# Kernel optimization log

Measured on AMD Instinct MI355X. Metric: run time of the kernel, lower is better.

The kernel has to match this reference:

```python
import jax, jax.numpy as jnp
import numpy as np

DIM = 2048
NUM_HEADS = 16
HEAD_DIM = DIM // NUM_HEADS  # 128


def setup_inputs() -> dict:
    key = jax.random.key(0)
    ks = jax.random.split(key, 5)
    scale = 0.02
    x = jax.random.normal(ks[0], (1, 2048, DIM), dtype=jnp.float32)
    # nn.Linear weights stored as [out_features, in_features]
    Wq = jax.random.normal(ks[1], (DIM, DIM), dtype=jnp.float32) * scale
    Wk = jax.random.normal(ks[2], (HEAD_DIM, DIM), dtype=jnp.float32) * scale
    Wv = jax.random.normal(ks[3], (HEAD_DIM, DIM), dtype=jnp.float32) * scale
    Wo = jax.random.normal(ks[4], (DIM, DIM), dtype=jnp.float32) * scale
    return {"x": x, "Wq": Wq, "Wk": Wk, "Wv": Wv, "Wo": Wo}


def reference(x, Wq, Wk, Wv, Wo):
    batch, seq_len, dim = x.shape
    q = x @ Wq.T                                   # [b, s, dim]
    k = x @ Wk.T                                   # [b, s, head_dim] (shared across heads)
    v = x @ Wv.T                                   # [b, s, head_dim]
    q = q.reshape(batch, seq_len, NUM_HEADS, HEAD_DIM).transpose(0, 2, 1, 3)  # [b, h, s, d]
    # MQA: single KV head broadcast across query heads (no materialized repeat)
    scores = jnp.einsum("bhqd,bkd->bhqk", q, k) / (HEAD_DIM ** 0.5)
    probs = jax.nn.softmax(scores, axis=-1)        # [b, h, q, k]
    out = jnp.einsum("bhqk,bkd->bhqd", probs, v)   # [b, h, s, d]
    out = out.transpose(0, 2, 1, 3).reshape(batch, seq_len, dim)
    return out @ Wo.T
```

## Files before the change

### kernel.cpp

```cpp
#include <hip/hip_runtime.h>
#include <cmath>

typedef float    float4_t __attribute__((ext_vector_type(4)));
typedef float    f32x16   __attribute__((ext_vector_type(16)));
typedef __bf16   bf16x8   __attribute__((ext_vector_type(8)));
typedef unsigned uint4_v  __attribute__((ext_vector_type(4)));
typedef unsigned short u16;

__device__ __forceinline__ u16 f2bf(float f) {
    unsigned u = __float_as_uint(f);
    u += 0x7fffu + ((u >> 16) & 1u);
    return (u16)(u >> 16);
}

__device__ __forceinline__ unsigned cvtpk(float a, float b) {
    unsigned r;
    asm("v_cvt_pk_bf16_f32 %0, %1, %2" : "=v"(r) : "v"(a), "v"(b));
    return r;
}
__device__ __forceinline__ void pl32swap(unsigned& a, unsigned& b) {
    asm volatile("v_permlane32_swap_b32 %0, %1" : "+v"(a), "+v"(b));
}

#define GLOAD_LDS16(g, l)                                              \
    __builtin_amdgcn_global_load_lds(                                  \
        (__attribute__((address_space(1))) void*)(g),                  \
        (__attribute__((address_space(3))) void*)(l), 16, 0, 0)

__device__ __forceinline__ int sw_st(int cs, int row) { return ((cs - (row >> 1)) & 3) * 8; }
__device__ __forceinline__ int sw_rd(int ch, int row) { return (((ch + (row >> 1)) & 3)) * 8; }

__global__ __launch_bounds__(256) void cast_all(const float* __restrict__ x,
                                                const float* __restrict__ wq,
                                                const float* __restrict__ wk,
                                                const float* __restrict__ wv,
                                                const float* __restrict__ wo,
                                                u16* __restrict__ xb, u16* __restrict__ wqb,
                                                u16* __restrict__ wkb, u16* __restrict__ wvb,
                                                u16* __restrict__ wob) {
    const int b = blockIdx.x;
    const float* src;
    u16* dst;
    int i;
    if (b < 4096)      { src = x;  dst = xb;  i = b * 256 + threadIdx.x; }
    else if (b < 8192) { src = wq; dst = wqb; i = (b - 4096) * 256 + threadIdx.x; }
    else if (b < 8448) { src = wk; dst = wkb; i = (b - 8192) * 256 + threadIdx.x; }
    else if (b < 8704) { src = wv; dst = wvb; i = (b - 8448) * 256 + threadIdx.x; }
    else               { src = wo; dst = wob; i = (b - 8704) * 256 + threadIdx.x; }
    float4 f = ((const float4*)src)[i];
    ushort4 r;
    r.x = f2bf(f.x); r.y = f2bf(f.y); r.z = f2bf(f.z); r.w = f2bf(f.w);
    ((ushort4*)dst)[i] = r;
}

template <typename EPI>
__device__ __forceinline__ void gemm_core(const u16* __restrict__ A,
                                          const u16* __restrict__ B,
                                          int K, int bm, int bn, EPI epi) {
    __shared__ __align__(16) u16 As[2][2 * 64 * 32];
    __shared__ __align__(16) u16 Bs[2][2 * 128 * 32];
    const int tid  = threadIdx.x;
    const int lane = tid & 63, wave = tid >> 6;
    const int quad = lane >> 4, l16 = lane & 15;

    float4_t acc[4][2] = {};

    auto stage = [&](int k0, int buf) {
#pragma unroll
        for (int i = 0; i < 2; ++i) {
            const int slot = i * 256 + tid;
            const int ksb = slot >> 8, win = slot & 255;
            const int row = win >> 2;
            GLOAD_LDS16(A + (size_t)(bm + row) * K + k0 + ksb * 32 + sw_st(win & 3, row),
                        &As[buf][slot * 8]);
        }
#pragma unroll
        for (int i = 0; i < 4; ++i) {
            const int slot = i * 256 + tid;
            const int ksb = slot >> 9, win = slot & 511;
            const int row = win >> 2;
            GLOAD_LDS16(B + (size_t)(bn + row) * K + k0 + ksb * 32 + sw_st(win & 3, row),
                        &Bs[buf][slot * 8]);
        }
    };

    stage(0, 0);
    __syncthreads();
    int cur = 0;
    for (int k0 = 0; k0 < K; k0 += 64) {
        if (k0 + 64 < K) stage(k0 + 64, cur ^ 1);

        bf16x8 af[2][4], bfr[2][2];
#pragma unroll
        for (int ksb = 0; ksb < 2; ++ksb) {
#pragma unroll
            for (int mi = 0; mi < 4; ++mi) {
                const int rw = mi * 16 + l16;
                af[ksb][mi] = *(const bf16x8*)&As[cur][ksb * 2048 + rw * 32 + sw_rd(quad, rw)];
            }
#pragma unroll
            for (int ni = 0; ni < 2; ++ni) {
                const int rw = wave * 32 + ni * 16 + l16;
                bfr[ksb][ni] = *(const bf16x8*)&Bs[cur][ksb * 4096 + rw * 32 + sw_rd(quad, rw)];
            }
        }
#pragma unroll
        for (int mi = 0; mi < 4; ++mi)
#pragma unroll
            for (int ni = 0; ni < 2; ++ni) {
                acc[mi][ni] = __builtin_amdgcn_mfma_f32_16x16x32_bf16(
                    af[0][mi], bfr[0][ni], acc[mi][ni], 0, 0, 0);
                acc[mi][ni] = __builtin_amdgcn_mfma_f32_16x16x32_bf16(
                    af[1][mi], bfr[1][ni], acc[mi][ni], 0, 0, 0);
            }
        __syncthreads();
        cur ^= 1;
    }

#pragma unroll
    for (int mi = 0; mi < 4; ++mi) {
        const int row = bm + mi * 16 + quad * 4;
#pragma unroll
        for (int ni = 0; ni < 2; ++ni) {
            const int col = bn + wave * 32 + ni * 16 + l16;
#pragma unroll
            for (int r = 0; r < 4; ++r) epi(row + r, col, acc[mi][ni][r]);
        }
    }
}

__global__ __launch_bounds__(256) void gemm_qkv(const u16* __restrict__ A,
                                                const u16* __restrict__ B,
                                                u16* __restrict__ qb,
                                                u16* __restrict__ kb,
                                                u16* __restrict__ vtb) {
    gemm_core(A, B, 2048, blockIdx.x * 64, blockIdx.y * 128,
              [=](int row, int col, float v) {
                  if (col < 2048)
                      qb[(size_t)row * 2048 + col] = f2bf(v * 0.1275174313451427f);
                  else if (col < 2176)
                      kb[(size_t)row * 128 + (col - 2048)] = f2bf(v);
                  else
                      vtb[(size_t)(col - 2176) * 2048 + row] = f2bf(v);
              });
}

__global__ __launch_bounds__(256) void gemm_out(const u16* __restrict__ A,
                                                const u16* __restrict__ B,
                                                float* __restrict__ C) {
    gemm_core(A, B, 2048, blockIdx.x * 64, blockIdx.y * 128,
              [=](int row, int col, float v) {
                  C[(size_t)row * 2048 + col] = v;
              });
}

__global__ __launch_bounds__(256) void mqa_attn(const u16* __restrict__ Q,
                                                const u16* __restrict__ Kmat,
                                                const u16* __restrict__ Vt,
                                                float* __restrict__ Oacc0,
                                                float* __restrict__ Oacc1,
                                                float* __restrict__ Lsum) {
    __shared__ __align__(16) u16 Ks[2][4 * 64 * 32];
    __shared__ __align__(16) u16 Vts[2][2 * 128 * 32];
    const int tid  = threadIdx.x;
    const int wave = tid >> 6, lane = tid & 63;
    const int l31 = lane & 31, hi = lane >> 5;
    const int h     = blockIdx.y;
    const int ksp   = blockIdx.z;
    const int qbase = blockIdx.x * 128 + wave * 32;
    const int kbase = ksp * 1024;

    bf16x8 qf[8];
    {
        const u16* qptr = Q + (size_t)(qbase + l31) * 2048 + h * 128 + hi * 8;
#pragma unroll
        for (int c = 0; c < 8; ++c) qf[c] = *(const bf16x8*)(qptr + c * 16);
    }

    f32x16 acc[4];
#pragma unroll
    for (int dt = 0; dt < 4; ++dt) acc[dt] = (f32x16)(0.0f);
    float lsum = 0.f;

    auto stage = [&](int s, int buf) {
        const int k0 = kbase + s * 64;
#pragma unroll
        for (int i = 0; i < 4; ++i) {
            const int slot = i * 256 + tid;
            const int kb4 = slot >> 8, win = slot & 255;
            const int row = win >> 2;
            GLOAD_LDS16(Kmat + (size_t)(k0 + row) * 128 + kb4 * 32 + sw_st(win & 3, row),
                        &Ks[buf][slot * 8]);
        }
#pragma unroll
        for (int i = 0; i < 4; ++i) {
            const int slot = i * 256 + tid;
            const int kk = slot >> 9, win = slot & 511;
            const int row = win >> 2;
            GLOAD_LDS16(Vt + (size_t)row * 2048 + k0 + kk * 32 + sw_st(win & 3, row),
                        &Vts[buf][slot * 8]);
        }
    };

    stage(0, 0);
    __syncthreads();
    int cur = 0;

    for (int s = 0; s < 16; ++s) {
        if (s < 15) stage(s + 1, cur ^ 1);

        bf16x8 pa[4];
#pragma unroll
        for (int kt = 0; kt < 2; ++kt) {
            f32x16 sv = (f32x16)(0.0f);
            const int row = kt * 32 + l31;
#pragma unroll
            for (int c = 0; c < 8; ++c) {
                const int ch = (c & 1) * 2 + hi;
                bf16x8 kf = *(const bf16x8*)&Ks[cur][(c >> 1) * 2048 + row * 32 + sw_rd(ch, row)];
                sv = __builtin_amdgcn_mfma_f32_32x32x16_bf16(kf, qf[c], sv, 0, 0, 0);
            }
            float e[16];
#pragma unroll
            for (int r = 0; r < 16; ++r) {
                e[r] = exp2f(sv[r]);
                lsum += e[r];
            }
#pragma unroll
            for (int half = 0; half < 2; ++half) {
                unsigned a0 = cvtpk(e[half * 8 + 0], e[half * 8 + 1]);
                unsigned a1 = cvtpk(e[half * 8 + 2], e[half * 8 + 3]);
                unsigned b0 = cvtpk(e[half * 8 + 4], e[half * 8 + 5]);
                unsigned b1 = cvtpk(e[half * 8 + 6], e[half * 8 + 7]);
                pl32swap(a0, b0);
                pl32swap(a1, b1);
                uint4_v w = {a0, a1, b0, b1};
                pa[kt * 2 + half] = __builtin_bit_cast(bf16x8, w);
            }
        }

#pragma unroll
        for (int kc = 0; kc < 4; ++kc) {
            const int ch = (kc & 1) * 2 + hi;
            const int kk = kc >> 1;
#pragma unroll
            for (int dt = 0; dt < 4; ++dt) {
                const int row = dt * 32 + l31;
                bf16x8 vf = *(const bf16x8*)&Vts[cur][kk * 4096 + row * 32 + sw_rd(ch, row)];
                acc[dt] = __builtin_amdgcn_mfma_f32_32x32x16_bf16(pa[kc], vf, acc[dt], 0, 0, 0);
            }
        }
        __syncthreads();
        cur ^= 1;
    }

    float lrow = lsum + __shfl_xor(lsum, 32);
    float* __restrict__ Op = ksp ? Oacc1 : Oacc0;
    if (lane < 32) Lsum[(size_t)ksp * 32768 + h * 2048 + qbase + l31] = lrow;
#pragma unroll
    for (int dt = 0; dt < 4; ++dt)
#pragma unroll
        for (int r = 0; r < 16; ++r) {
            const int qloc = (r & 3) + 8 * (r >> 2) + 4 * hi;
            Op[((size_t)h * 2048 + qbase + qloc) * 128 + dt * 32 + l31] = acc[dt][r];
        }
}

__global__ __launch_bounds__(256) void attn_combine(const float* __restrict__ O0,
                                                    const float* __restrict__ O1,
                                                    const float* __restrict__ L,
                                                    u16* __restrict__ attn) {
    const int f = blockIdx.x * 256 + threadIdx.x;
    const int d4 = f & 31, h = (f >> 5) & 15, q = f >> 9;
    const int li = h * 2048 + q;
    const float inv = 1.0f / (L[li] + L[32768 + li]);
    const int oi = li * 32 + d4;
    const float4 a = ((const float4*)O0)[oi];
    const float4 b = ((const float4*)O1)[oi];
    ushort4 r;
    r.x = f2bf((a.x + b.x) * inv);
    r.y = f2bf((a.y + b.y) * inv);
    r.z = f2bf((a.z + b.z) * inv);
    r.w = f2bf((a.w + b.w) * inv);
    ((ushort4*)attn)[f] = r;
}

extern "C" void kernel_launch(void* const* d_in, const int* in_sizes, int n_in,
                              void* d_out, int out_size, void* d_ws, size_t ws_size,
                              hipStream_t stream) {
    const float* x  = (const float*)d_in[0];
    const float* Wq = (const float*)d_in[1];
    const float* Wk = (const float*)d_in[2];
    const float* Wv = (const float*)d_in[3];
    const float* Wo = (const float*)d_in[4];
    float* out = (float*)d_out;

    u16* ws   = (u16*)d_ws;
    u16* xb   = ws;
    u16* Wqb  = xb  + (4 << 20);
    u16* Wkb  = Wqb + (4 << 20);
    u16* Wvb  = Wkb + (256 << 10);
    u16* Wob  = Wvb + (256 << 10);
    u16* qb   = Wob + (4 << 20);
    u16* kb   = qb  + (4 << 20);
    u16* vtb  = kb  + (256 << 10);
    u16* attn = vtb + (256 << 10);
    float* Oacc0 = (float*)ws;
    float* Oacc1 = (float*)(attn + (4 << 20));
    float* Lsum  = Oacc1 + (4 << 20);

    cast_all<<<12800, 256, 0, stream>>>(x, Wq, Wk, Wv, Wo, xb, Wqb, Wkb, Wvb, Wob);

    gemm_qkv<<<dim3(32, 18), 256, 0, stream>>>(xb, Wqb, qb, kb, vtb);
    mqa_attn<<<dim3(16, 16, 2), 256, 0, stream>>>(qb, kb, vtb, Oacc0, Oacc1, Lsum);
    attn_combine<<<4096, 256, 0, stream>>>(Oacc0, Oacc1, Lsum, attn);
    gemm_out<<<dim3(32, 16), 256, 0, stream>>>(attn, Wob, out);
}
```

Baseline: 219.0 us.

## Read K and V^T directly from global memory in MQA attention, dropping LDS staging

The attention kernel no longer stages K and V^T tiles through double-buffered shared memory with barriers. Each wave instead loads its MFMA operands straight from global memory, relying on L2/cache reuse since the single shared KV head is small. V^T is written with a padded row stride (2112) so that strided global reads avoid channel or bank conflicts, and the workspace is enlarged to fit it. This removes LDS traffic and __syncthreads, but exposes global-load latency with no explicit prefetch beyond unrolling by two.

New measurement: 309.5 us. 1.41x slower.

```diff
diff --git a/kernel.cpp b/kernel.cpp
--- a/kernel.cpp
+++ b/kernel.cpp
@@ -6,6 +6,8 @@
 typedef __bf16   bf16x8   __attribute__((ext_vector_type(8)));
 typedef unsigned uint4_v  __attribute__((ext_vector_type(4)));
 typedef unsigned short u16;
+
+#define VSTR 2112
 
 __device__ __forceinline__ u16 f2bf(float f) {
     unsigned u = __float_as_uint(f);
@@ -141,7 +143,7 @@
                   else if (col < 2176)
                       kb[(size_t)row * 128 + (col - 2048)] = f2bf(v);
                   else
-                      vtb[(size_t)(col - 2176) * 2048 + row] = f2bf(v);
+                      vtb[(size_t)(col - 2176) * VSTR + row] = f2bf(v);
               });
 }
 
@@ -160,8 +162,6 @@
                                                 float* __restrict__ Oacc0,
                                                 float* __restrict__ Oacc1,
                                                 float* __restrict__ Lsum) {
-    __shared__ __align__(16) u16 Ks[2][4 * 64 * 32];
-    __shared__ __align__(16) u16 Vts[2][2 * 128 * 32];
     const int tid  = threadIdx.x;
     const int wave = tid >> 6, lane = tid & 63;
     const int l31 = lane & 31, hi = lane >> 5;
@@ -182,42 +182,18 @@
     for (int dt = 0; dt < 4; ++dt) acc[dt] = (f32x16)(0.0f);
     float lsum = 0.f;
 
-    auto stage = [&](int s, int buf) {
+#pragma unroll 2
+    for (int s = 0; s < 16; ++s) {
         const int k0 = kbase + s * 64;
-#pragma unroll
-        for (int i = 0; i < 4; ++i) {
-            const int slot = i * 256 + tid;
-            const int kb4 = slot >> 8, win = slot & 255;
-            const int row = win >> 2;
-            GLOAD_LDS16(Kmat + (size_t)(k0 + row) * 128 + kb4 * 32 + sw_st(win & 3, row),
-                        &Ks[buf][slot * 8]);
-        }
-#pragma unroll
-        for (int i = 0; i < 4; ++i) {
-            const int slot = i * 256 + tid;
-            const int kk = slot >> 9, win = slot & 511;
-            const int row = win >> 2;
-            GLOAD_LDS16(Vt + (size_t)row * 2048 + k0 + kk * 32 + sw_st(win & 3, row),
-                        &Vts[buf][slot * 8]);
-        }
-    };
-
-    stage(0, 0);
-    __syncthreads();
-    int cur = 0;
-
-    for (int s = 0; s < 16; ++s) {
-        if (s < 15) stage(s + 1, cur ^ 1);
 
         bf16x8 pa[4];
 #pragma unroll
         for (int kt = 0; kt < 2; ++kt) {
             f32x16 sv = (f32x16)(0.0f);
-            const int row = kt * 32 + l31;
+            const u16* kp = Kmat + (size_t)(k0 + kt * 32 + l31) * 128 + hi * 8;
 #pragma unroll
             for (int c = 0; c < 8; ++c) {
-                const int ch = (c & 1) * 2 + hi;
-                bf16x8 kf = *(const bf16x8*)&Ks[cur][(c >> 1) * 2048 + row * 32 + sw_rd(ch, row)];
+                bf16x8 kf = *(const bf16x8*)(kp + c * 16);
                 sv = __builtin_amdgcn_mfma_f32_32x32x16_bf16(kf, qf[c], sv, 0, 0, 0);
             }
             float e[16];
@@ -240,18 +216,14 @@
         }
 
 #pragma unroll
-        for (int kc = 0; kc < 4; ++kc) {
-            const int ch = (kc & 1) * 2 + hi;
-            const int kk = kc >> 1;
-#pragma unroll
-            for (int dt = 0; dt < 4; ++dt) {
-                const int row = dt * 32 + l31;
-                bf16x8 vf = *(const bf16x8*)&Vts[cur][kk * 4096 + row * 32 + sw_rd(ch, row)];
+        for (int dt = 0; dt < 4; ++dt) {
+            const u16* vp = Vt + (size_t)(dt * 32 + l31) * VSTR + k0 + hi * 8;
+#pragma unroll
+            for (int kc = 0; kc < 4; ++kc) {
+                bf16x8 vf = *(const bf16x8*)(vp + kc * 16);
                 acc[dt] = __builtin_amdgcn_mfma_f32_32x32x16_bf16(pa[kc], vf, acc[dt], 0, 0, 0);
             }
         }
-        __syncthreads();
-        cur ^= 1;
     }
 
     float lrow = lsum + __shfl_xor(lsum, 32);
@@ -304,7 +276,7 @@
     u16* qb   = Wob + (4 << 20);
     u16* kb   = qb  + (4 << 20);
     u16* vtb  = kb  + (256 << 10);
-    u16* attn = vtb + (256 << 10);
+    u16* attn = vtb + (512 << 10);
     float* Oacc0 = (float*)ws;
     float* Oacc1 = (float*)(attn + (4 << 20));
     float* Lsum  = Oacc1 + (4 << 20);
```

## Process two query tiles per wave in MQA attention and pad V^T stride

Applied to the files above, without the earlier changes.

Each wave now handles 64 query rows (two 32-row tiles) instead of 32, so every K and V fragment read from LDS feeds two MFMAs. The block shrinks to 128 threads (2 waves) while keeping the same 128-query tile, and staging loops are doubled to compensate. V^T rows are padded to a stride of 2112 to reduce channel/bank conflicts on the global loads. This roughly doubles register pressure per wave (accumulators and Q fragments) and halves waves per block, which risks lower occupancy and less latency hiding.

After: 238.7 us. +9.0%, slower.

```diff
diff --git a/kernel.cpp b/kernel.cpp
--- a/kernel.cpp
+++ b/kernel.cpp
@@ -6,6 +6,8 @@
 typedef __bf16   bf16x8   __attribute__((ext_vector_type(8)));
 typedef unsigned uint4_v  __attribute__((ext_vector_type(4)));
 typedef unsigned short u16;
+
+#define VSTR 2112
 
 __device__ __forceinline__ u16 f2bf(float f) {
     unsigned u = __float_as_uint(f);
@@ -141,7 +143,7 @@
                   else if (col < 2176)
                       kb[(size_t)row * 128 + (col - 2048)] = f2bf(v);
                   else
-                      vtb[(size_t)(col - 2176) * 2048 + row] = f2bf(v);
+                      vtb[(size_t)(col - 2176) * VSTR + row] = f2bf(v);
               });
 }
 
@@ -154,12 +156,12 @@
               });
 }
 
-__global__ __launch_bounds__(256) void mqa_attn(const u16* __restrict__ Q,
-                                                const u16* __restrict__ Kmat,
-                                                const u16* __restrict__ Vt,
-                                                float* __restrict__ Oacc0,
-                                                float* __restrict__ Oacc1,
-                                                float* __restrict__ Lsum) {
+__global__ __launch_bounds__(128, 1) void mqa_attn(const u16* __restrict__ Q,
+                                                   const u16* __restrict__ Kmat,
+                                                   const u16* __restrict__ Vt,
+                                                   float* __restrict__ Oacc0,
+                                                   float* __restrict__ Oacc1,
+                                                   float* __restrict__ Lsum) {
     __shared__ __align__(16) u16 Ks[2][4 * 64 * 32];
     __shared__ __align__(16) u16 Vts[2][2 * 128 * 32];
     const int tid  = threadIdx.x;
@@ -167,37 +169,40 @@
     const int l31 = lane & 31, hi = lane >> 5;
     const int h     = blockIdx.y;
     const int ksp   = blockIdx.z;
-    const int qbase = blockIdx.x * 128 + wave * 32;
+    const int qbase = blockIdx.x * 128 + wave * 64;
     const int kbase = ksp * 1024;
 
-    bf16x8 qf[8];
-    {
-        const u16* qptr = Q + (size_t)(qbase + l31) * 2048 + h * 128 + hi * 8;
-#pragma unroll
-        for (int c = 0; c < 8; ++c) qf[c] = *(const bf16x8*)(qptr + c * 16);
-    }
-
-    f32x16 acc[4];
-#pragma unroll
-    for (int dt = 0; dt < 4; ++dt) acc[dt] = (f32x16)(0.0f);
-    float lsum = 0.f;
+    bf16x8 qf[2][8];
+#pragma unroll
+    for (int qt = 0; qt < 2; ++qt) {
+        const u16* qptr = Q + (size_t)(qbase + qt * 32 + l31) * 2048 + h * 128 + hi * 8;
+#pragma unroll
+        for (int c = 0; c < 8; ++c) qf[qt][c] = *(const bf16x8*)(qptr + c * 16);
+    }
+
+    f32x16 acc[2][4];
+#pragma unroll
+    for (int qt = 0; qt < 2; ++qt)
+#pragma unroll
+        for (int dt = 0; dt < 4; ++dt) acc[qt][dt] = (f32x16)(0.0f);
+    float ls0 = 0.f, ls1 = 0.f;
 
     auto stage = [&](int s, int buf) {
         const int k0 = kbase + s * 64;
 #pragma unroll
-        for (int i = 0; i < 4; ++i) {
-            const int slot = i * 256 + tid;
+        for (int i = 0; i < 8; ++i) {
+            const int slot = i * 128 + tid;
             const int kb4 = slot >> 8, win = slot & 255;
             const int row = win >> 2;
             GLOAD_LDS16(Kmat + (size_t)(k0 + row) * 128 + kb4 * 32 + sw_st(win & 3, row),
                         &Ks[buf][slot * 8]);
         }
 #pragma unroll
-        for (int i = 0; i < 4; ++i) {
-            const int slot = i * 256 + tid;
+        for (int i = 0; i < 8; ++i) {
+            const int slot = i * 128 + tid;
             const int kk = slot >> 9, win = slot & 511;
             const int row = win >> 2;
-            GLOAD_LDS16(Vt + (size_t)row * 2048 + k0 + kk * 32 + sw_st(win & 3, row),
+            GLOAD_LDS16(Vt + (size_t)row * VSTR + k0 + kk * 32 + sw_st(win & 3, row),
                         &Vts[buf][slot * 8]);
         }
     };
@@ -209,33 +214,43 @@
     for (int s = 0; s < 16; ++s) {
         if (s < 15) stage(s + 1, cur ^ 1);
 
-        bf16x8 pa[4];
+        bf16x8 pa[2][4];
 #pragma unroll
         for (int kt = 0; kt < 2; ++kt) {
-            f32x16 sv = (f32x16)(0.0f);
+            f32x16 sv0 = (f32x16)(0.0f), sv1 = (f32x16)(0.0f);
             const int row = kt * 32 + l31;
 #pragma unroll
             for (int c = 0; c < 8; ++c) {
-                const int ch = (c & 1) * 2 + hi;
-                bf16x8 kf = *(const bf16x8*)&Ks[cur][(c >> 1) * 2048 + row * 32 + sw_rd(ch, row)];
-                sv = __builtin_amdgcn_mfma_f32_32x32x16_bf16(kf, qf[c], sv, 0, 0, 0);
-            }
-            float e[16];
+                bf16x8 kf = *(const bf16x8*)&Ks[cur][(c >> 1) * 2048 + row * 32 +
+                                                    sw_rd((c & 1) * 2 + hi, row)];
+                sv0 = __builtin_amdgcn_mfma_f32_32x32x16_bf16(kf, qf[0][c], sv0, 0, 0, 0);
+                sv1 = __builtin_amdgcn_mfma_f32_32x32x16_bf16(kf, qf[1][c], sv1, 0, 0, 0);
+            }
+            float e0[16], e1[16];
 #pragma unroll
             for (int r = 0; r < 16; ++r) {
-                e[r] = exp2f(sv[r]);
-                lsum += e[r];
+                e0[r] = exp2f(sv0[r]); ls0 += e0[r];
+                e1[r] = exp2f(sv1[r]); ls1 += e1[r];
             }
 #pragma unroll
             for (int half = 0; half < 2; ++half) {
-                unsigned a0 = cvtpk(e[half * 8 + 0], e[half * 8 + 1]);
-                unsigned a1 = cvtpk(e[half * 8 + 2], e[half * 8 + 3]);
-                unsigned b0 = cvtpk(e[half * 8 + 4], e[half * 8 + 5]);
-                unsigned b1 = cvtpk(e[half * 8 + 6], e[half * 8 + 7]);
+                unsigned a0 = cvtpk(e0[half * 8 + 0], e0[half * 8 + 1]);
+                unsigned a1 = cvtpk(e0[half * 8 + 2], e0[half * 8 + 3]);
+                unsigned b0 = cvtpk(e0[half * 8 + 4], e0[half * 8 + 5]);
+                unsigned b1 = cvtpk(e0[half * 8 + 6], e0[half * 8 + 7]);
                 pl32swap(a0, b0);
                 pl32swap(a1, b1);
-                uint4_v w = {a0, a1, b0, b1};
-                pa[kt * 2 + half] = __builtin_bit_cast(bf16x8, w);
+                uint4_v w0 = {a0, a1, b0, b1};
+                pa[0][kt * 2 + half] = __builtin_bit_cast(bf16x8, w0);
+
+                unsigned c0 = cvtpk(e1[half * 8 + 0], e1[half * 8 + 1]);
+                unsigned c1 = cvtpk(e1[half * 8 + 2], e1[half * 8 + 3]);
+                unsigned d0 = cvtpk(e1[half * 8 + 4], e1[half * 8 + 5]);
+                unsigned d1 = cvtpk(e1[half * 8 + 6], e1[half * 8 + 7]);
+                pl32swap(c0, d0);
+                pl32swap(c1, d1);
+                uint4_v w1 = {c0, c1, d0, d1};
+                pa[1][kt * 2 + half] = __builtin_bit_cast(bf16x8, w1);
             }
         }
 
@@ -247,23 +262,30 @@
             for (int dt = 0; dt < 4; ++dt) {
                 const int row = dt * 32 + l31;
                 bf16x8 vf = *(const bf16x8*)&Vts[cur][kk * 4096 + row * 32 + sw_rd(ch, row)];
-                acc[dt] = __builtin_amdgcn_mfma_f32_32x32x16_bf16(pa[kc], vf, acc[dt], 0, 0, 0);
+                acc[0][dt] = __builtin_amdgcn_mfma_f32_32x32x16_bf16(pa[0][kc], vf, acc[0][dt], 0, 0, 0);
+                acc[1][dt] = __builtin_amdgcn_mfma_f32_32x32x16_bf16(pa[1][kc], vf, acc[1][dt], 0, 0, 0);
             }
         }
         __syncthreads();
         cur ^= 1;
     }
 
-    float lrow = lsum + __shfl_xor(lsum, 32);
     float* __restrict__ Op = ksp ? Oacc1 : Oacc0;
-    if (lane < 32) Lsum[(size_t)ksp * 32768 + h * 2048 + qbase + l31] = lrow;
-#pragma unroll
-    for (int dt = 0; dt < 4; ++dt)
-#pragma unroll
-        for (int r = 0; r < 16; ++r) {
-            const int qloc = (r & 3) + 8 * (r >> 2) + 4 * hi;
-            Op[((size_t)h * 2048 + qbase + qloc) * 128 + dt * 32 + l31] = acc[dt][r];
-        }
+#pragma unroll
+    for (int qt = 0; qt < 2; ++qt) {
+        float lrow = qt ? ls1 : ls0;
+        lrow += __shfl_xor(lrow, 32);
+        if (lane < 32)
+            Lsum[(size_t)ksp * 32768 + h * 2048 + qbase + qt * 32 + l31] = lrow;
+#pragma unroll
+        for (int dt = 0; dt < 4; ++dt)
+#pragma unroll
+            for (int r = 0; r < 16; ++r) {
+                const int qloc = (r & 3) + 8 * (r >> 2) + 4 * hi;
+                Op[((size_t)h * 2048 + qbase + qt * 32 + qloc) * 128 + dt * 32 + l31] =
+                    acc[qt][dt][r];
+            }
+    }
 }
 
 __global__ __launch_bounds__(256) void attn_combine(const float* __restrict__ O0,
@@ -304,7 +326,7 @@
     u16* qb   = Wob + (4 << 20);
     u16* kb   = qb  + (4 << 20);
     u16* vtb  = kb  + (256 << 10);
-    u16* attn = vtb + (256 << 10);
+    u16* attn = vtb + (512 << 10);
     float* Oacc0 = (float*)ws;
     float* Oacc1 = (float*)(attn + (4 << 20));
     float* Lsum  = Oacc1 + (4 << 20);
@@ -312,7 +334,7 @@
     cast_all<<<12800, 256, 0, stream>>>(x, Wq, Wk, Wv, Wo, xb, Wqb, Wkb, Wvb, Wob);
 
     gemm_qkv<<<dim3(32, 18), 256, 0, stream>>>(xb, Wqb, qb, kb, vtb);
-    mqa_attn<<<dim3(16, 16, 2), 256, 0, stream>>>(qb, kb, vtb, Oacc0, Oacc1, Lsum);
+    mqa_attn<<<dim3(16, 16, 2), 128, 0, stream>>>(qb, kb, vtb, Oacc0, Oacc1, Lsum);
     attn_combine<<<4096, 256, 0, stream>>>(Oacc0, Oacc1, Lsum, attn);
     gemm_out<<<dim3(32, 16), 256, 0, stream>>>(attn, Wob, out);
 }
```
